# Performance work log

Measured on AMD Instinct MI355X. Metric: run time of the kernel, lower is better.

Reference implementation:

```python
import jax, jax.numpy as jnp
import numpy as np

NUM_EXPERTS = 8
TOP_K = 2
N_EMBD = 1024
D_FFN = 2048  # 4*n_embd//top_k, already multiple of block_size=128


def setup_inputs() -> dict:
    key = jax.random.key(0)
    k1, k2, k3, k4 = jax.random.split(key, 4)
    x = jax.random.normal(k1, (4, 2048, N_EMBD), dtype=jnp.float32)
    router_w = jax.random.normal(k2, (NUM_EXPERTS, N_EMBD), dtype=jnp.float32) * 0.02
    w1 = jax.random.normal(k3, (N_EMBD, D_FFN * NUM_EXPERTS), dtype=jnp.float32) * 0.02
    w2 = jax.random.normal(k4, (D_FFN * NUM_EXPERTS, N_EMBD), dtype=jnp.float32) * 0.02
    return {"x": x, "router_w": router_w, "w1": w1, "w2": w2}


def reference(x, router_w, w1, w2):
    B, T, D = x.shape
    xf = x.reshape(B * T, D)                       # [N, d]
    N = B * T

    # Router: softmax over experts, then top-k selection and renormalization.
    logits = xf @ router_w.T                       # [N, E]
    probs = jax.nn.softmax(logits, axis=-1)
    top_v, top_i = jax.lax.top_k(probs, TOP_K)     # [N, k]
    top_v = top_v / jnp.sum(top_v, axis=-1, keepdims=True)  # norm_topk_prob=True

    # Dense [N, E] routing-weight matrix (zero for non-selected experts).
    gate = jnp.zeros((N, NUM_EXPERTS), dtype=x.dtype)
    gate = gate.at[jnp.arange(N)[:, None], top_i].set(top_v)

    w1r = w1.reshape(D, NUM_EXPERTS, D_FFN)        # expert-major column blocks
    w2r = w2.reshape(NUM_EXPERTS, D_FFN, D)

    out = jnp.zeros((N, D), dtype=x.dtype)
    for e in range(NUM_EXPERTS):
        h = jax.nn.gelu(xf @ w1r[:, e, :], approximate=False)  # [N, f]
        out = out + gate[:, e:e + 1] * (h @ w2r[e])
    return out.reshape(B, T, D)
```

## Files before the change

kernel.cpp:

```cpp
#include <hip/hip_runtime.h>
#include <hip/hip_bf16.h>
#include <cstdint>
#include <cstddef>

#define NE 8
#define N_TOK 8192
#define D_EMB 1024
#define D_FFN 2048

#define BM 128
#define BN 128
#define BK 32

typedef __attribute__((ext_vector_type(8))) short short8;
typedef __attribute__((ext_vector_type(4))) float f32x4;

__device__ __forceinline__ unsigned short f2bf(float f) {
  union { float f; unsigned int u; } c; c.f = f;
  unsigned int u = c.u;
  unsigned int r = u + 0x7FFFu + ((u >> 16) & 1u);
  return (unsigned short)(r >> 16);
}

__device__ __forceinline__ float bf2f(unsigned short u) {
  union { unsigned int u; float f; } c; c.u = ((unsigned int)u) << 16;
  return c.f;
}

__device__ __forceinline__ void gll16(const void* g, void* l) {
  __builtin_amdgcn_global_load_lds((const __attribute__((address_space(1))) void*)g,
                                   (__attribute__((address_space(3))) void*)l, 16, 0, 0);
}

__global__ __launch_bounds__(256) void router_k(const float* __restrict__ x,
                                                const float* __restrict__ rw,
                                                int* __restrict__ ti,
                                                float* __restrict__ tg,
                                                ushort* __restrict__ xb) {
  int w = threadIdx.x >> 6, lane = threadIdx.x & 63;
  int n = blockIdx.x * 4 + w;
  const float4* x4 = (const float4*)(x + (size_t)n * D_EMB);
  ushort4* xb4 = (ushort4*)(xb + (size_t)n * D_EMB);
  const float4* r4 = (const float4*)rw;
  float acc[NE];
#pragma unroll
  for (int e = 0; e < NE; ++e) acc[e] = 0.f;
#pragma unroll
  for (int c = 0; c < 4; ++c) {
    float4 xv = x4[c * 64 + lane];
    ushort4 o;
    o.x = f2bf(xv.x); o.y = f2bf(xv.y); o.z = f2bf(xv.z); o.w = f2bf(xv.w);
    xb4[c * 64 + lane] = o;
#pragma unroll
    for (int e = 0; e < NE; ++e) {
      float4 wv = r4[e * 256 + c * 64 + lane];
      acc[e] += xv.x * wv.x + xv.y * wv.y + xv.z * wv.z + xv.w * wv.w;
    }
  }
#pragma unroll
  for (int e = 0; e < NE; ++e) {
    float v = acc[e];
#pragma unroll
    for (int off = 32; off >= 1; off >>= 1) v += __shfl_xor(v, off);
    acc[e] = v;
  }
  if (lane == 0) {
    int e0 = 0; float v0 = acc[0];
#pragma unroll
    for (int e = 1; e < NE; ++e) if (acc[e] > v0) { v0 = acc[e]; e0 = e; }
    int e1 = -1; float v1 = -1e30f;
#pragma unroll
    for (int e = 0; e < NE; ++e) if (e != e0 && acc[e] > v1) { v1 = acc[e]; e1 = e; }
    float p1 = expf(v1 - v0);
    float g0 = 1.f / (1.f + p1);
    float g1 = p1 * g0;
    ti[2 * n] = e0; ti[2 * n + 1] = e1;
    tg[2 * n] = g0; tg[2 * n + 1] = g1;
  }
}

__global__ __launch_bounds__(256) void hist_k(const int* __restrict__ ti,
                                              int* __restrict__ counts) {
  __shared__ int lc[NE];
  if (threadIdx.x < NE) lc[threadIdx.x] = 0;
  __syncthreads();
  int s = blockIdx.x * 512 + threadIdx.x;
  atomicAdd(&lc[ti[s]], 1);
  atomicAdd(&lc[ti[s + 256]], 1);
  __syncthreads();
  if (threadIdx.x < NE) atomicAdd(&counts[threadIdx.x], lc[threadIdx.x]);
}

__global__ void prefix_k(const int* __restrict__ counts, int* __restrict__ bases,
                         int* __restrict__ cursor) {
  if (threadIdx.x == 0) {
    int s = 0;
    for (int e = 0; e < NE; ++e) { bases[e] = s; cursor[e] = s; s += counts[e]; }
  }
}

__global__ __launch_bounds__(256) void scatter_k(const int* __restrict__ ti,
                                                 const float* __restrict__ tg,
                                                 int* __restrict__ cursor,
                                                 int* __restrict__ tok,
                                                 float* __restrict__ gate,
                                                 int* __restrict__ inv) {
  __shared__ int lc[NE], lb[NE];
  if (threadIdx.x < NE) lc[threadIdx.x] = 0;
  __syncthreads();
  int s = blockIdx.x * 256 + threadIdx.x;
  int e = ti[s];
  float g = tg[s];
  int loc = atomicAdd(&lc[e], 1);
  __syncthreads();
  if (threadIdx.x < NE) lb[threadIdx.x] = atomicAdd(&cursor[threadIdx.x], lc[threadIdx.x]);
  __syncthreads();
  int pos = lb[e] + loc;
  tok[pos] = s >> 1;
  gate[pos] = g;
  inv[s] = pos;
}

__global__ __launch_bounds__(256) void transpose_bf_k(const float* __restrict__ src,
                                                      ushort* __restrict__ dst,
                                                      int R, int C) {
  __shared__ ushort t[32][33];
  int bx = blockIdx.x, by = blockIdx.y;
  int rl = threadIdx.x >> 3, q = threadIdx.x & 7;
  float4 v = *(const float4*)&src[(size_t)(by * 32 + rl) * C + bx * 32 + q * 4];
  t[rl][q * 4 + 0] = f2bf(v.x);
  t[rl][q * 4 + 1] = f2bf(v.y);
  t[rl][q * 4 + 2] = f2bf(v.z);
  t[rl][q * 4 + 3] = f2bf(v.w);
  __syncthreads();
  ushort4 o;
  o.x = t[q * 4 + 0][rl];
  o.y = t[q * 4 + 1][rl];
  o.z = t[q * 4 + 2][rl];
  o.w = t[q * 4 + 3][rl];
  *(ushort4*)&dst[(size_t)(bx * 32 + rl) * R + by * 32 + q * 4] = o;
}


__global__ __launch_bounds__(256) void gemm1_k(const ushort* __restrict__ xb,
                                               const ushort* __restrict__ w1t,
                                               const int* __restrict__ counts,
                                               const int* __restrict__ bases,
                                               const int* __restrict__ tok,
                                               ushort* __restrict__ h) {
  int bid = (int)blockIdx.x;
  bid = (bid & 7) * (NE * 1024 / 8) + (bid >> 3);
  int e = bid >> 10;
  int rem = bid & 1023;
  int mt = rem >> 4, nt = rem & 15;
  int count = counts[e];
  if (mt * BM >= count) return;
  int base = bases[e];

  __shared__ ushort Al[BM * BK];
  __shared__ ushort Bl[BN * BK];

  int tid = threadIdx.x;
  int w = tid >> 6, lane = tid & 63;

  const int ssw = (((lane & 3) ^ ((lane >> 3) & 3))) * 8;

  const ushort* aptr[2]; const ushort* bptr[2];
  ushort* alds[2]; ushort* blds[2];
#pragma unroll
  for (int j = 0; j < 2; ++j) {
    int rl = w * 32 + j * 16 + (lane >> 2);
    int pr = min(base + mt * BM + rl, base + count - 1);
    int t = tok[pr];
    aptr[j] = xb + (size_t)t * D_EMB + ssw;
    int c = e * D_FFN + nt * BN + rl;
    bptr[j] = w1t + (size_t)c * D_EMB + ssw;
    alds[j] = Al + (w * 32 + j * 16) * BK;
    blds[j] = Bl + (w * 32 + j * 16) * BK;
  }

  f32x4 zero = {0.f, 0.f, 0.f, 0.f};
  f32x4 acc[4][4];
#pragma unroll
  for (int i = 0; i < 4; ++i)
#pragma unroll
    for (int j = 0; j < 4; ++j) acc[i][j] = zero;

  int wm = w >> 1, wn = w & 1;
  const int rsw = ((lane >> 4) ^ (((lane & 15) >> 1) & 3)) * 8;
  const int arow = (wm * 64 + (lane & 15)) * BK + rsw;
  const int brow = (wn * 64 + (lane & 15)) * BK + rsw;

  for (int ks = 0; ks < D_EMB / BK; ++ks) {
    __syncthreads();
#pragma unroll
    for (int j = 0; j < 2; ++j) {
      gll16(aptr[j], alds[j]);
      gll16(bptr[j], blds[j]);
      aptr[j] += BK; bptr[j] += BK;
    }
    __syncthreads();
    short8 a[4], b[4];
#pragma unroll
    for (int i = 0; i < 4; ++i) a[i] = *(const short8*)&Al[arow + i * 16 * BK];
#pragma unroll
    for (int j = 0; j < 4; ++j) b[j] = *(const short8*)&Bl[brow + j * 16 * BK];
#pragma unroll
    for (int i = 0; i < 4; ++i)
#pragma unroll
      for (int j = 0; j < 4; ++j)
        acc[i][j] = __builtin_amdgcn_mfma_f32_16x16x32_bf16(a[i], b[j], acc[i][j], 0, 0, 0);
  }

  int r0 = mt * BM + wm * 64, c0 = nt * BN + wn * 64;
#pragma unroll
  for (int i = 0; i < 4; ++i) {
#pragma unroll
    for (int q = 0; q < 4; ++q) {
      int row = r0 + i * 16 + (lane >> 4) * 4 + q;
      if (row < count) {
        size_t hb = (size_t)(base + row) * D_FFN;
#pragma unroll
        for (int j = 0; j < 4; ++j) {
          float v = acc[i][j][q];
          v = 0.5f * v * (1.f + erff(v * 0.70710678118654752f));
          h[hb + c0 + j * 16 + (lane & 15)] = f2bf(v);
        }
      }
    }
  }
}

__global__ __launch_bounds__(256) void gemm2_k(const ushort* __restrict__ h,
                                               const ushort* __restrict__ w2t,
                                               const int* __restrict__ counts,
                                               const int* __restrict__ bases,
                                               const int* __restrict__ tok,
                                               const float* __restrict__ gate,
                                               ushort* __restrict__ y) {
  int bid = (int)blockIdx.x;
  bid = (bid & 7) * (NE * 512 / 8) + (bid >> 3);
  int e = bid >> 9;
  int rem = bid & 511;
  int mt = rem >> 3, nt = rem & 7;
  int count = counts[e];
  if (mt * BM >= count) return;
  int base = bases[e];

  __shared__ ushort Al[BM * BK];
  __shared__ ushort Bl[BN * BK];

  int tid = threadIdx.x;
  int w = tid >> 6, lane = tid & 63;

  const int ssw = (((lane & 3) ^ ((lane >> 3) & 3))) * 8;

  const ushort* aptr[2]; const ushort* bptr[2];
  ushort* alds[2]; ushort* blds[2];
#pragma unroll
  for (int j = 0; j < 2; ++j) {
    int rl = w * 32 + j * 16 + (lane >> 2);
    int pr = min(base + mt * BM + rl, base + count - 1);
    aptr[j] = h + (size_t)pr * D_FFN + ssw;
    int d = nt * BN + rl;
    bptr[j] = w2t + (size_t)d * (NE * D_FFN) + e * D_FFN + ssw;
    alds[j] = Al + (w * 32 + j * 16) * BK;
    blds[j] = Bl + (w * 32 + j * 16) * BK;
  }

  f32x4 zero = {0.f, 0.f, 0.f, 0.f};
  f32x4 acc[4][4];
#pragma unroll
  for (int i = 0; i < 4; ++i)
#pragma unroll
    for (int j = 0; j < 4; ++j) acc[i][j] = zero;

  int wm = w >> 1, wn = w & 1;
  const int rsw = ((lane >> 4) ^ (((lane & 15) >> 1) & 3)) * 8;
  const int arow = (wm * 64 + (lane & 15)) * BK + rsw;
  const int brow = (wn * 64 + (lane & 15)) * BK + rsw;

  for (int ks = 0; ks < D_FFN / BK; ++ks) {
    __syncthreads();
#pragma unroll
    for (int j = 0; j < 2; ++j) {
      gll16(aptr[j], alds[j]);
      gll16(bptr[j], blds[j]);
      aptr[j] += BK; bptr[j] += BK;
    }
    __syncthreads();
    short8 a[4], b[4];
#pragma unroll
    for (int i = 0; i < 4; ++i) a[i] = *(const short8*)&Al[arow + i * 16 * BK];
#pragma unroll
    for (int j = 0; j < 4; ++j) b[j] = *(const short8*)&Bl[brow + j * 16 * BK];
#pragma unroll
    for (int i = 0; i < 4; ++i)
#pragma unroll
      for (int j = 0; j < 4; ++j)
        acc[i][j] = __builtin_amdgcn_mfma_f32_16x16x32_bf16(a[i], b[j], acc[i][j], 0, 0, 0);
  }

  int r0 = mt * BM + wm * 64, c0 = nt * BN + wn * 64;
#pragma unroll
  for (int i = 0; i < 4; ++i) {
#pragma unroll
    for (int q = 0; q < 4; ++q) {
      int row = r0 + i * 16 + (lane >> 4) * 4 + q;
      if (row < count) {
        int pr = base + row;
        float g = gate[pr];
        size_t yb = (size_t)pr * D_EMB;
#pragma unroll
        for (int j = 0; j < 4; ++j) {
          y[yb + c0 + j * 16 + (lane & 15)] = f2bf(g * acc[i][j][q]);
        }
      }
    }
  }
}

__global__ __launch_bounds__(256) void combine_k(const ushort* __restrict__ y,
                                                 const int* __restrict__ inv,
                                                 float* __restrict__ out) {
  int n = blockIdx.x;
  int p0 = inv[2 * n], p1 = inv[2 * n + 1];
  const ushort4* r0 = (const ushort4*)(y + (size_t)p0 * D_EMB);
  const ushort4* r1 = (const ushort4*)(y + (size_t)p1 * D_EMB);
  float4* o = (float4*)(out + (size_t)n * D_EMB);
  int i = threadIdx.x;
  ushort4 a = r0[i], b = r1[i];
  float4 v;
  v.x = bf2f(a.x) + bf2f(b.x);
  v.y = bf2f(a.y) + bf2f(b.y);
  v.z = bf2f(a.z) + bf2f(b.z);
  v.w = bf2f(a.w) + bf2f(b.w);
  o[i] = v;
}

extern "C" void kernel_launch(void* const* d_in, const int* in_sizes, int n_in,
                              void* d_out, int out_size, void* d_ws, size_t ws_size,
                              hipStream_t stream) {
  const float* x  = (const float*)d_in[0];
  const float* rw = (const float*)d_in[1];
  const float* w1 = (const float*)d_in[2];
  const float* w2 = (const float*)d_in[3];
  float* out = (float*)d_out;

  char* ws = (char*)d_ws;
  size_t off = 0;
  auto alloc = [&](size_t bytes) {
    void* p = ws + off;
    off = (off + bytes + 255) & ~(size_t)255;
    return p;
  };
  int*    counts = (int*)alloc(32);
  int*    bases  = (int*)alloc(32);
  int*    cursor = (int*)alloc(32);
  int*    ti     = (int*)alloc((size_t)N_TOK * 2 * sizeof(int));
  float*  tg     = (float*)alloc((size_t)N_TOK * 2 * sizeof(float));
  int*    tok    = (int*)alloc((size_t)N_TOK * 2 * sizeof(int));
  float*  gate   = (float*)alloc((size_t)N_TOK * 2 * sizeof(float));
  int*    inv    = (int*)alloc((size_t)N_TOK * 2 * sizeof(int));
  ushort* xb     = (ushort*)alloc((size_t)N_TOK * D_EMB * 2);
  ushort* w1t    = (ushort*)alloc((size_t)D_EMB * NE * D_FFN * 2);
  ushort* w2t    = (ushort*)alloc((size_t)D_EMB * NE * D_FFN * 2);
  ushort* hbuf   = (ushort*)alloc((size_t)N_TOK * 2 * D_FFN * 2);
  ushort* ybuf   = (ushort*)alloc((size_t)N_TOK * 2 * D_EMB * 2);
  (void)ws_size; (void)in_sizes; (void)n_in; (void)out_size;

  hipMemsetAsync(counts, 0, 32, stream);

  router_k<<<N_TOK / 4, 256, 0, stream>>>(x, rw, ti, tg, xb);
  transpose_bf_k<<<dim3(512, 32), 256, 0, stream>>>(w1, w1t, D_EMB, NE * D_FFN);
  transpose_bf_k<<<dim3(32, 512), 256, 0, stream>>>(w2, w2t, NE * D_FFN, D_EMB);
  hist_k<<<N_TOK * 2 / 512, 256, 0, stream>>>(ti, counts);
  prefix_k<<<1, 64, 0, stream>>>(counts, bases, cursor);
  scatter_k<<<N_TOK * 2 / 256, 256, 0, stream>>>(ti, tg, cursor, tok, gate, inv);
  gemm1_k<<<NE * 64 * 16, 256, 0, stream>>>(xb, w1t, counts, bases, tok, hbuf);
  gemm2_k<<<NE * 64 * 8, 256, 0, stream>>>(hbuf, w2t, counts, bases, tok, gate, ybuf);
  combine_k<<<N_TOK, 256, 0, stream>>>(ybuf, inv, out);
}
```

Measured before the change: 284.6 us.

## Double-buffer GEMM k-loops, use fast sigmoid GELU, scatter gemm2 output by token slot

Both expert GEMMs now use two LDS buffers, issuing the next global-to-LDS load before computing on the current tile, with explicit vmcnt waits and barriers. This overlaps memory latency with MFMA work. The exact erf GELU is replaced with a tanh-style sigmoid approximation using exp and rcp, which costs less in the epilogue but deviates slightly from the exact reference. The scatter now stores the original slot index, so gemm2 writes each row to its token-slot position and combine reads contiguous rows, dropping the inverse-index buffer.

```diff
diff --git a/kernel.cpp b/kernel.cpp
--- a/kernel.cpp
+++ b/kernel.cpp
@@ -27,10 +27,20 @@
   return c.f;
 }
 
+__device__ __forceinline__ float gelu_f(float x) {
+  float u = x * x * x * 0.044715f + x;
+  float t = __expf(-1.5957691216057308f * u);
+  return x * __builtin_amdgcn_rcpf(1.f + t);
+}
+
 __device__ __forceinline__ void gll16(const void* g, void* l) {
   __builtin_amdgcn_global_load_lds((const __attribute__((address_space(1))) void*)g,
                                    (__attribute__((address_space(3))) void*)l, 16, 0, 0);
 }
+
+#define SB() __builtin_amdgcn_sched_barrier(0)
+#define VW(N) { asm volatile("s_waitcnt vmcnt(" #N ")" ::: "memory"); SB(); }
+#define BAR() { SB(); __builtin_amdgcn_s_barrier(); SB(); }
 
 __global__ __launch_bounds__(256) void router_k(const float* __restrict__ x,
                                                 const float* __restrict__ rw,
@@ -102,9 +112,8 @@
 __global__ __launch_bounds__(256) void scatter_k(const int* __restrict__ ti,
                                                  const float* __restrict__ tg,
                                                  int* __restrict__ cursor,
-                                                 int* __restrict__ tok,
-                                                 float* __restrict__ gate,
-                                                 int* __restrict__ inv) {
+                                                 int* __restrict__ tokS,
+                                                 float* __restrict__ gate) {
   __shared__ int lc[NE], lb[NE];
   if (threadIdx.x < NE) lc[threadIdx.x] = 0;
   __syncthreads();
@@ -116,9 +125,8 @@
   if (threadIdx.x < NE) lb[threadIdx.x] = atomicAdd(&cursor[threadIdx.x], lc[threadIdx.x]);
   __syncthreads();
   int pos = lb[e] + loc;
-  tok[pos] = s >> 1;
+  tokS[pos] = s;
   gate[pos] = g;
-  inv[s] = pos;
 }
 
 __global__ __launch_bounds__(256) void transpose_bf_k(const float* __restrict__ src,
@@ -142,11 +150,38 @@
 }
 
 
+#define STG(BUF)                                                           \
+  { _Pragma("unroll") for (int j_ = 0; j_ < 2; ++j_) {                     \
+      gll16(aptr[j_], &Al[BUF][ldso[j_]]);                                 \
+      gll16(bptr[j_], &Bl[BUF][ldso[j_]]);                                 \
+      aptr[j_] += BK; bptr[j_] += BK;                                      \
+    } }
+
+#define CMP(BUF)                                                           \
+  { short8 a[4], b[4];                                                     \
+    _Pragma("unroll") for (int i_ = 0; i_ < 4; ++i_)                       \
+      a[i_] = *(const short8*)&Al[BUF][arow + i_ * 16 * BK];               \
+    _Pragma("unroll") for (int j_ = 0; j_ < 4; ++j_)                       \
+      b[j_] = *(const short8*)&Bl[BUF][brow + j_ * 16 * BK];               \
+    _Pragma("unroll") for (int i_ = 0; i_ < 4; ++i_)                       \
+      _Pragma("unroll") for (int j_ = 0; j_ < 4; ++j_)                     \
+        acc[i_][j_] = __builtin_amdgcn_mfma_f32_16x16x32_bf16(a[i_], b[j_], acc[i_][j_], 0, 0, 0); \
+  }
+
+#define KLOOP(NT)                                                          \
+  STG(0);                                                                  \
+  for (int ks = 0; ks < (NT) - 2; ks += 2) {                               \
+    STG(1); VW(4); BAR(); CMP(0); BAR();                                   \
+    STG(0); VW(4); BAR(); CMP(1); BAR();                                   \
+  }                                                                        \
+  STG(1); VW(4); BAR(); CMP(0); BAR();                                     \
+  VW(0); BAR(); CMP(1);
+
 __global__ __launch_bounds__(256) void gemm1_k(const ushort* __restrict__ xb,
                                                const ushort* __restrict__ w1t,
                                                const int* __restrict__ counts,
                                                const int* __restrict__ bases,
-                                               const int* __restrict__ tok,
+                                               const int* __restrict__ tokS,
                                                ushort* __restrict__ h) {
   int bid = (int)blockIdx.x;
   bid = (bid & 7) * (NE * 1024 / 8) + (bid >> 3);
@@ -157,8 +192,8 @@
   if (mt * BM >= count) return;
   int base = bases[e];
 
-  __shared__ ushort Al[BM * BK];
-  __shared__ ushort Bl[BN * BK];
+  __shared__ ushort Al[2][BM * BK];
+  __shared__ ushort Bl[2][BN * BK];
 
   int tid = threadIdx.x;
   int w = tid >> 6, lane = tid & 63;
@@ -166,17 +201,16 @@
   const int ssw = (((lane & 3) ^ ((lane >> 3) & 3))) * 8;
 
   const ushort* aptr[2]; const ushort* bptr[2];
-  ushort* alds[2]; ushort* blds[2];
+  int ldso[2];
 #pragma unroll
   for (int j = 0; j < 2; ++j) {
     int rl = w * 32 + j * 16 + (lane >> 2);
     int pr = min(base + mt * BM + rl, base + count - 1);
-    int t = tok[pr];
+    int t = tokS[pr] >> 1;
     aptr[j] = xb + (size_t)t * D_EMB + ssw;
     int c = e * D_FFN + nt * BN + rl;
     bptr[j] = w1t + (size_t)c * D_EMB + ssw;
-    alds[j] = Al + (w * 32 + j * 16) * BK;
-    blds[j] = Bl + (w * 32 + j * 16) * BK;
+    ldso[j] = (w * 32 + j * 16) * BK;
   }
 
   f32x4 zero = {0.f, 0.f, 0.f, 0.f};
@@ -191,26 +225,7 @@
   const int arow = (wm * 64 + (lane & 15)) * BK + rsw;
   const int brow = (wn * 64 + (lane & 15)) * BK + rsw;
 
-  for (int ks = 0; ks < D_EMB / BK; ++ks) {
-    __syncthreads();
-#pragma unroll
-    for (int j = 0; j < 2; ++j) {
-      gll16(aptr[j], alds[j]);
-      gll16(bptr[j], blds[j]);
-      aptr[j] += BK; bptr[j] += BK;
-    }
-    __syncthreads();
-    short8 a[4], b[4];
-#pragma unroll
-    for (int i = 0; i < 4; ++i) a[i] = *(const short8*)&Al[arow + i * 16 * BK];
-#pragma unroll
-    for (int j = 0; j < 4; ++j) b[j] = *(const short8*)&Bl[brow + j * 16 * BK];
-#pragma unroll
-    for (int i = 0; i < 4; ++i)
-#pragma unroll
-      for (int j = 0; j < 4; ++j)
-        acc[i][j] = __builtin_amdgcn_mfma_f32_16x16x32_bf16(a[i], b[j], acc[i][j], 0, 0, 0);
-  }
+  KLOOP(D_EMB / BK);
 
   int r0 = mt * BM + wm * 64, c0 = nt * BN + wn * 64;
 #pragma unroll
@@ -222,9 +237,7 @@
         size_t hb = (size_t)(base + row) * D_FFN;
 #pragma unroll
         for (int j = 0; j < 4; ++j) {
-          float v = acc[i][j][q];
-          v = 0.5f * v * (1.f + erff(v * 0.70710678118654752f));
-          h[hb + c0 + j * 16 + (lane & 15)] = f2bf(v);
+          h[hb + c0 + j * 16 + (lane & 15)] = f2bf(gelu_f(acc[i][j][q]));
         }
       }
     }
@@ -235,9 +248,9 @@
                                                const ushort* __restrict__ w2t,
                                                const int* __restrict__ counts,
                                                const int* __restrict__ bases,
-                                               const int* __restrict__ tok,
+                                               const int* __restrict__ tokS,
                                                const float* __restrict__ gate,
-                                               ushort* __restrict__ y) {
+                                               ushort* __restrict__ y2) {
   int bid = (int)blockIdx.x;
   bid = (bid & 7) * (NE * 512 / 8) + (bid >> 3);
   int e = bid >> 9;
@@ -247,8 +260,8 @@
   if (mt * BM >= count) return;
   int base = bases[e];
 
-  __shared__ ushort Al[BM * BK];
-  __shared__ ushort Bl[BN * BK];
+  __shared__ ushort Al[2][BM * BK];
+  __shared__ ushort Bl[2][BN * BK];
 
   int tid = threadIdx.x;
   int w = tid >> 6, lane = tid & 63;
@@ -256,7 +269,7 @@
   const int ssw = (((lane & 3) ^ ((lane >> 3) & 3))) * 8;
 
   const ushort* aptr[2]; const ushort* bptr[2];
-  ushort* alds[2]; ushort* blds[2];
+  int ldso[2];
 #pragma unroll
   for (int j = 0; j < 2; ++j) {
     int rl = w * 32 + j * 16 + (lane >> 2);
@@ -264,8 +277,7 @@
     aptr[j] = h + (size_t)pr * D_FFN + ssw;
     int d = nt * BN + rl;
     bptr[j] = w2t + (size_t)d * (NE * D_FFN) + e * D_FFN + ssw;
-    alds[j] = Al + (w * 32 + j * 16) * BK;
-    blds[j] = Bl + (w * 32 + j * 16) * BK;
+    ldso[j] = (w * 32 + j * 16) * BK;
   }
 
   f32x4 zero = {0.f, 0.f, 0.f, 0.f};
@@ -280,26 +292,7 @@
   const int arow = (wm * 64 + (lane & 15)) * BK + rsw;
   const int brow = (wn * 64 + (lane & 15)) * BK + rsw;
 
-  for (int ks = 0; ks < D_FFN / BK; ++ks) {
-    __syncthreads();
-#pragma unroll
-    for (int j = 0; j < 2; ++j) {
-      gll16(aptr[j], alds[j]);
-      gll16(bptr[j], blds[j]);
-      aptr[j] += BK; bptr[j] += BK;
-    }
-    __syncthreads();
-    short8 a[4], b[4];
-#pragma unroll
-    for (int i = 0; i < 4; ++i) a[i] = *(const short8*)&Al[arow + i * 16 * BK];
-#pragma unroll
-    for (int j = 0; j < 4; ++j) b[j] = *(const short8*)&Bl[brow + j * 16 * BK];
-#pragma unroll
-    for (int i = 0; i < 4; ++i)
-#pragma unroll
-      for (int j = 0; j < 4; ++j)
-        acc[i][j] = __builtin_amdgcn_mfma_f32_16x16x32_bf16(a[i], b[j], acc[i][j], 0, 0, 0);
-  }
+  KLOOP(D_FFN / BK);
 
   int r0 = mt * BM + wm * 64, c0 = nt * BN + wn * 64;
 #pragma unroll
@@ -310,23 +303,21 @@
       if (row < count) {
         int pr = base + row;
         float g = gate[pr];
-        size_t yb = (size_t)pr * D_EMB;
+        size_t yb = (size_t)tokS[pr] * D_EMB;
 #pragma unroll
         for (int j = 0; j < 4; ++j) {
-          y[yb + c0 + j * 16 + (lane & 15)] = f2bf(g * acc[i][j][q]);
+          y2[yb + c0 + j * 16 + (lane & 15)] = f2bf(g * acc[i][j][q]);
         }
       }
     }
   }
 }
 
-__global__ __launch_bounds__(256) void combine_k(const ushort* __restrict__ y,
-                                                 const int* __restrict__ inv,
+__global__ __launch_bounds__(256) void combine_k(const ushort* __restrict__ y2,
                                                  float* __restrict__ out) {
   int n = blockIdx.x;
-  int p0 = inv[2 * n], p1 = inv[2 * n + 1];
-  const ushort4* r0 = (const ushort4*)(y + (size_t)p0 * D_EMB);
-  const ushort4* r1 = (const ushort4*)(y + (size_t)p1 * D_EMB);
+  const ushort4* r0 = (const ushort4*)(y2 + (size_t)(2 * n) * D_EMB);
+  const ushort4* r1 = (const ushort4*)(y2 + (size_t)(2 * n + 1) * D_EMB);
   float4* o = (float4*)(out + (size_t)n * D_EMB);
   int i = threadIdx.x;
   ushort4 a = r0[i], b = r1[i];
@@ -359,9 +350,8 @@
   int*    cursor = (int*)alloc(32);
   int*    ti     = (int*)alloc((size_t)N_TOK * 2 * sizeof(int));
   float*  tg     = (float*)alloc((size_t)N_TOK * 2 * sizeof(float));
-  int*    tok    = (int*)alloc((size_t)N_TOK * 2 * sizeof(int));
+  int*    tokS   = (int*)alloc((size_t)N_TOK * 2 * sizeof(int));
   float*  gate   = (float*)alloc((size_t)N_TOK * 2 * sizeof(float));
-  int*    inv    = (int*)alloc((size_t)N_TOK * 2 * sizeof(int));
   ushort* xb     = (ushort*)alloc((size_t)N_TOK * D_EMB * 2);
   ushort* w1t    = (ushort*)alloc((size_t)D_EMB * NE * D_FFN * 2);
   ushort* w2t    = (ushort*)alloc((size_t)D_EMB * NE * D_FFN * 2);
@@ -376,8 +366,8 @@
   transpose_bf_k<<<dim3(32, 512), 256, 0, stream>>>(w2, w2t, NE * D_FFN, D_EMB);
   hist_k<<<N_TOK * 2 / 512, 256, 0, stream>>>(ti, counts);
   prefix_k<<<1, 64, 0, stream>>>(counts, bases, cursor);
-  scatter_k<<<N_TOK * 2 / 256, 256, 0, stream>>>(ti, tg, cursor, tok, gate, inv);
-  gemm1_k<<<NE * 64 * 16, 256, 0, stream>>>(xb, w1t, counts, bases, tok, hbuf);
-  gemm2_k<<<NE * 64 * 8, 256, 0, stream>>>(hbuf, w2t, counts, bases, tok, gate, ybuf);
-  combine_k<<<N_TOK, 256, 0, stream>>>(ybuf, inv, out);
-}
+  scatter_k<<<N_TOK * 2 / 256, 256, 0, stream>>>(ti, tg, cursor, tokS, gate);
+  gemm1_k<<<NE * 64 * 16, 256, 0, stream>>>(xb, w1t, counts, bases, tokS, hbuf);
+  gemm2_k<<<NE * 64 * 8, 256, 0, stream>>>(hbuf, w2t, counts, bases, tokS, gate, ybuf);
+  combine_k<<<N_TOK, 256, 0, stream>>>(ybuf, out);
+}
```

After: 281.8 us. No clear change (-1.0%).
